# Kernel tuning notes

Hardware: AMD Instinct MI355X
Metric: run time of the kernel (lower is better)

## Reference

```python
import jax, jax.numpy as jnp
import numpy as np

N = 50000      # nodes
E = 800000     # edges
FEAT = 128     # node_feat_size
HID = 128      # hidden_channels
LAT = 64       # latent_size
G = 256        # number of graphs in the batch


def _glorot_like(key, fan_in, shape):
    s = 1.0 / np.sqrt(fan_in)
    return jax.random.uniform(key, shape, jnp.float32, -s, s)


def setup_inputs() -> dict:
    key = jax.random.key(0)
    ks = jax.random.split(key, 13)
    x = jax.random.normal(ks[0], (N, FEAT), jnp.float32)
    edge_index = jax.random.randint(ks[1], (2, E), 0, N, dtype=jnp.int64)
    batch = jnp.sort(jax.random.randint(ks[2], (N,), 0, G, dtype=jnp.int64))
    return {
        "x": x,
        "edge_index": edge_index,
        "batch": batch,
        # GCNConv1: FEAT -> HID
        "W1": _glorot_like(ks[3], FEAT, (FEAT, HID)), "b1": jnp.zeros((HID,), jnp.float32),
        # GCNConv2: HID -> HID
        "W2": _glorot_like(ks[4], HID, (HID, HID)), "b2": jnp.zeros((HID,), jnp.float32),
        # fc: HID -> LAT
        "fcW": _glorot_like(ks[5], HID, (HID, LAT)), "fcb": _glorot_like(ks[6], HID, (LAT,)),
        # decoder: LAT -> HID
        "decW": _glorot_like(ks[7], LAT, (LAT, HID)), "decb": _glorot_like(ks[8], LAT, (HID,)),
        # GCNConv3: HID -> FEAT
        "W3": _glorot_like(ks[9], HID, (HID, FEAT)), "b3": jnp.zeros((FEAT,), jnp.float32),
    }


def reference(x, edge_index, batch, W1, b1, W2, b2, fcW, fcb, decW, decb, W3, b3):
    # --- GCN normalization with self-loops (computed once, shared by all convs) ---
    loop = jnp.arange(N, dtype=edge_index.dtype)
    row = jnp.concatenate([edge_index[0], loop])   # source nodes [E+N]
    col = jnp.concatenate([edge_index[1], loop])   # target nodes [E+N]
    deg = jax.ops.segment_sum(jnp.ones(row.shape, x.dtype), col, num_segments=N)
    dinv = jnp.where(deg > 0, jax.lax.rsqrt(deg), jnp.zeros_like(deg))
    norm = dinv[row] * dinv[col]                   # [E+N]

    def gcn(h, W, b):
        h = h @ W                                   # [N, out] transform first (PyG order)
        msg = h[row] * norm[:, None]                # gather + scale, [E+N, out]
        out = jax.ops.segment_sum(msg, col, num_segments=N)  # scatter-add
        return out + b

    # --- encode ---
    h = jax.nn.relu(gcn(x, W1, b1))
    h = jax.nn.relu(gcn(h, W2, b2))
    pooled = jax.ops.segment_sum(h, batch, num_segments=G)   # global_add_pool [G, HID]
    latent = jax.nn.relu(pooled @ fcW + fcb)                 # [G, LAT]

    # --- decode ---
    z = jax.nn.relu(latent @ decW + decb)                    # [G, HID]
    z = z[batch]                                             # broadcast back to nodes [N, HID]
    recon = gcn(z, W3, b3)                                   # [N, FEAT]
    return recon, latent
```

## Files before the change

kernel.cpp:

```cpp
#include <hip/hip_runtime.h>
#include <hip/hip_fp16.h>

static constexpr int NN   = 50000;
static constexpr int EE   = 800000;
static constexpr int GG   = 256;
static constexpr int PCH  = 16;
static constexpr int BK   = 128;
static constexpr int NB   = (NN + BK - 1) / BK;
static constexpr int CAP  = 4096;
static constexpr int CH   = 2048;
static constexpr int ABLK = (EE + CH - 1) / CH;
static constexpr int PBBB = EE / 64;

typedef _Float16 f16;
typedef f16  f16x8 __attribute__((ext_vector_type(8)));
typedef float f32x4 __attribute__((ext_vector_type(4)));

__device__ __forceinline__ int lowerb(const int* __restrict__ b, int n, int v) {
    int lo = 0, hi = n;
    while (lo < hi) { int m = (lo + hi) >> 1; if (b[m] < v) lo = m + 1; else hi = m; }
    return lo;
}

__device__ __forceinline__ int pack_rec(int bg, float w) {
    __half h = __float2half(w);
    return bg | ((int)__builtin_bit_cast(unsigned short, h) << 16);
}
__device__ __forceinline__ float rec_w(int rec) {
    return __half2float(__builtin_bit_cast(__half, (unsigned short)((unsigned)rec >> 16)));
}

__global__ __launch_bounds__(256) void prep_k(const float* __restrict__ W1,
                                              const float* __restrict__ W2,
                                              f16x8* __restrict__ whi1, f16x8* __restrict__ wlo1,
                                              f16x8* __restrict__ whi2, f16x8* __restrict__ wlo2,
                                              int* __restrict__ bcur,
                                              float* __restrict__ pooled)
{
    int blk = blockIdx.x, t = threadIdx.x;
    if (blk < 16) {
        const float* W = (blk < 8) ? W1 : W2;
        f16x8* wh = (blk < 8) ? whi1 : whi2;
        f16x8* wl = (blk < 8) ? wlo1 : wlo2;
        int tid = (blk & 7) * 256 + t;
        int m  = tid & 15;
        int kq = (tid >> 4) & 3;
        int ks = (tid >> 6) & 3;
        int nt = tid >> 8;
        int n  = nt * 16 + m;
        int k0 = ks * 32 + kq * 8;
        f16x8 h8, l8;
        #pragma unroll
        for (int u = 0; u < 8; u++) {
            float x = W[(size_t)(k0 + u) * 128 + n];
            f16 h = (f16)x;
            h8[u] = h;
            l8[u] = (f16)(x - (float)h);
        }
        wh[tid] = h8;
        wl[tid] = l8;
    } else if (blk == 16) {
        for (int b = t; b < NB; b += 256) bcur[b] = b * CAP;
    } else {
        float4* p = (float4*)pooled;
        for (int j = (blk - 17) * 256 + t; j < GG * 32; j += 512)
            p[j] = make_float4(0.f, 0.f, 0.f, 0.f);
    }
}

__global__ __launch_bounds__(512) void binA_k(const int* __restrict__ ei,
                                              int* __restrict__ bcur,
                                              int2* __restrict__ eraw)
{
    __shared__ int2  stage[CH];
    __shared__ short sbid[CH];
    __shared__ int   hist[NB], loff[NB], gbase[NB], lcur[NB];
    __shared__ int   sc[512];

    int tid = threadIdx.x;
    int e0 = blockIdx.x * CH;
    int n = EE - e0; if (n > CH) n = CH;

    for (int b = tid; b < NB; b += 512) hist[b] = 0;
    __syncthreads();

    int2 r[CH / 512];
    #pragma unroll
    for (int k = 0; k < CH / 512; k++) {
        int s = k * 512 + tid;
        if (s < n) {
            int src = ei[e0 + s];
            int dst = ei[EE + e0 + s];
            r[k] = make_int2(src, dst);
            atomicAdd(&hist[dst >> 7], 1);
        }
    }
    __syncthreads();
    int v = (tid < NB) ? hist[tid] : 0;
    sc[tid] = v;
    __syncthreads();
    #pragma unroll
    for (int off = 1; off < 512; off <<= 1) {
        int add = (tid >= off) ? sc[tid - off] : 0;
        __syncthreads();
        sc[tid] += add;
        __syncthreads();
    }
    if (tid < NB) { int ex = sc[tid] - v; loff[tid] = ex; lcur[tid] = ex; }
    __syncthreads();
    for (int b = tid; b < NB; b += 512)
        gbase[b] = atomicAdd(&bcur[b], hist[b]);
    __syncthreads();
    #pragma unroll
    for (int k = 0; k < CH / 512; k++) {
        int s = k * 512 + tid;
        if (s < n) {
            int b = r[k].y >> 7;
            int slot = atomicAdd(&lcur[b], 1);
            stage[slot] = r[k];
            sbid[slot]  = (short)b;
        }
    }
    __syncthreads();
    for (int s = tid; s < n; s += 512) {
        int b = sbid[s];
        eraw[(size_t)gbase[b] + (s - loff[b])] = stage[s];
    }
}

__global__ __launch_bounds__(512) void binB_k(const int2* __restrict__ eraw,
                                              const int* __restrict__ bcur,
                                              int* __restrict__ rowptr,
                                              float* __restrict__ dinv,
                                              int* __restrict__ ebuf)
{
    __shared__ int hist[BK], excl[BK], cur[BK];
    __shared__ int red[512];
    int b = blockIdx.x, tid = threadIdx.x;
    int t0 = b << 7;
    int lim = NN - t0; if (lim > BK) lim = BK;
    int tot = bcur[b] - b * CAP;

    red[tid] = (tid < b) ? (bcur[tid] - tid * CAP) : 0;
    __syncthreads();
    #pragma unroll
    for (int off = 256; off > 0; off >>= 1) {
        if (tid < off) red[tid] += red[tid + off];
        __syncthreads();
    }
    int base = red[0];
    __syncthreads();

    const int2* er = eraw + (size_t)b * CAP;

    if (tid < BK) hist[tid] = 0;
    __syncthreads();
    for (int s = tid; s < tot; s += 512) atomicAdd(&hist[er[s].y & 127], 1);
    __syncthreads();
    if (tid < BK) excl[tid] = hist[tid];
    __syncthreads();
    #pragma unroll
    for (int off = 1; off < BK; off <<= 1) {
        int add = (tid >= off && tid < BK) ? excl[tid - off] : 0;
        __syncthreads();
        if (tid < BK) excl[tid] += add;
        __syncthreads();
    }
    if (tid < BK) {
        int ex = excl[tid] - hist[tid];
        cur[tid] = base + ex;
        if (tid < lim) {
            rowptr[t0 + tid] = base + ex;
            dinv[t0 + tid]   = rsqrtf((float)(hist[tid] + 1));
        }
    }
    if (b == NB - 1 && tid == 0) rowptr[NN] = EE;
    __syncthreads();
    for (int s = tid; s < tot; s += 512) {
        int2 rec = er[s];
        int p = atomicAdd(&cur[rec.y & 127], 1);
        ebuf[p] = rec.x;
    }
}

__global__ __launch_bounds__(512) void gemm_mfma3_k(const float* __restrict__ in,
                                                    const f16x8* __restrict__ whi_f,
                                                    const f16x8* __restrict__ wlo_f,
                                                    const float* __restrict__ dinv,
                                                    __half* __restrict__ out,
                                                    int rows)
{
    __shared__ __align__(16) f16x8 sh[2048];
    int tid  = threadIdx.x;
    #pragma unroll
    for (int u = 0; u < 4; u++) sh[u * 512 + tid] = whi_f[u * 512 + tid];
    __syncthreads();

    int lane = tid & 63;
    int wv   = tid >> 6;
    int rB   = blockIdx.x * 128 + wv * 16;
    int m    = lane & 15;
    int kq   = lane >> 4;
    int r    = rB + m;
    int rr   = (r < rows) ? r : (rows - 1);

    f16x8 ahi[4], alo[4];
    const float* rp = in + (size_t)rr * 128 + kq * 8;
    #pragma unroll
    for (int ks = 0; ks < 4; ks++) {
        float4 p0 = *(const float4*)(rp + ks * 32);
        float4 p1 = *(const float4*)(rp + ks * 32 + 4);
        float xs[8] = {p0.x, p0.y, p0.z, p0.w, p1.x, p1.y, p1.z, p1.w};
        #pragma unroll
        for (int u = 0; u < 8; u++) {
            f16 h = (f16)xs[u];
            ahi[ks][u] = h;
            alo[ks][u] = (f16)(xs[u] - (float)h);
        }
    }

    f32x4 acc[8];
    #pragma unroll
    for (int n = 0; n < 8; n++) acc[n] = (f32x4){0.f, 0.f, 0.f, 0.f};

    #pragma unroll
    for (int nt = 0; nt < 8; nt++) {
        #pragma unroll
        for (int ks = 0; ks < 4; ks++) {
            int idx = ((nt * 4 + ks) * 4 + kq) * 16 + m;
            f16x8 bh = sh[idx];
            f16x8 bl = wlo_f[idx];
            acc[nt] = __builtin_amdgcn_mfma_f32_16x16x32_f16(ahi[ks], bh, acc[nt], 0, 0, 0);
            acc[nt] = __builtin_amdgcn_mfma_f32_16x16x32_f16(alo[ks], bh, acc[nt], 0, 0, 0);
            acc[nt] = __builtin_amdgcn_mfma_f32_16x16x32_f16(ahi[ks], bl, acc[nt], 0, 0, 0);
        }
    }

    int   orow[4];
    float dv[4];
    #pragma unroll
    for (int j = 0; j < 4; j++) {
        int gr = rB + kq * 4 + j;
        orow[j] = gr;
        dv[j]   = (gr < rows) ? dinv[gr] : 0.f;
    }
    #pragma unroll
    for (int nt = 0; nt < 8; nt++) {
        int c = nt * 16 + m;
        #pragma unroll
        for (int j = 0; j < 4; j++) {
            if (orow[j] < rows)
                out[(size_t)orow[j] * 128 + c] = __float2half(acc[nt][j] * dv[j]);
        }
    }
}

__global__ __launch_bounds__(512) void gemm_mfma2h_k(const __half* __restrict__ in,
                                                     const f16x8* __restrict__ whi_f,
                                                     const f16x8* __restrict__ wlo_f,
                                                     const float* __restrict__ dinv,
                                                     __half* __restrict__ out,
                                                     int rows)
{
    __shared__ __align__(16) f16x8 sh[2048];
    int tid  = threadIdx.x;
    #pragma unroll
    for (int u = 0; u < 4; u++) sh[u * 512 + tid] = whi_f[u * 512 + tid];
    __syncthreads();

    int lane = tid & 63;
    int wv   = tid >> 6;
    int rB   = blockIdx.x * 128 + wv * 16;
    int m    = lane & 15;
    int kq   = lane >> 4;
    int r    = rB + m;
    int rr   = (r < rows) ? r : (rows - 1);

    f16x8 ah[4];
    const f16* rp = (const f16*)in + (size_t)rr * 128 + kq * 8;
    #pragma unroll
    for (int ks = 0; ks < 4; ks++)
        ah[ks] = *(const f16x8*)(rp + ks * 32);

    f32x4 acc[8];
    #pragma unroll
    for (int n = 0; n < 8; n++) acc[n] = (f32x4){0.f, 0.f, 0.f, 0.f};

    #pragma unroll
    for (int nt = 0; nt < 8; nt++) {
        #pragma unroll
        for (int ks = 0; ks < 4; ks++) {
            int idx = ((nt * 4 + ks) * 4 + kq) * 16 + m;
            f16x8 bh = sh[idx];
            f16x8 bl = wlo_f[idx];
            acc[nt] = __builtin_amdgcn_mfma_f32_16x16x32_f16(ah[ks], bh, acc[nt], 0, 0, 0);
            acc[nt] = __builtin_amdgcn_mfma_f32_16x16x32_f16(ah[ks], bl, acc[nt], 0, 0, 0);
        }
    }

    int   orow[4];
    float dv[4];
    #pragma unroll
    for (int j = 0; j < 4; j++) {
        int gr = rB + kq * 4 + j;
        orow[j] = gr;
        dv[j]   = (gr < rows) ? dinv[gr] : 0.f;
    }
    #pragma unroll
    for (int nt = 0; nt < 8; nt++) {
        int c = nt * 16 + m;
        #pragma unroll
        for (int j = 0; j < 4; j++) {
            if (orow[j] < rows)
                out[(size_t)orow[j] * 128 + c] = __float2half(acc[nt][j] * dv[j]);
        }
    }
}

__device__ __forceinline__ float4 gat4h(const __half* __restrict__ t, int s, int q)
{
    uint2 v = *(const uint2*)(t + ((size_t)s << 7) + q * 4);
    __half2 a = __builtin_bit_cast(__half2, v.x);
    __half2 b = __builtin_bit_cast(__half2, v.y);
    float2 fa = __half22float2(a), fb = __half22float2(b);
    return make_float4(fa.x, fa.y, fb.x, fb.y);
}

#define AGG_BODY                                                                 \
    int e0 = __builtin_amdgcn_readfirstlane(rowptr[i]);                          \
    int e1 = __builtin_amdgcn_readfirstlane(rowptr[i + 1]);                      \
    int deg = e1 - e0;                                                           \
    int idxsafe = (deg > 0) ? (e0 + min(lane, deg - 1)) : 0;                     \
    int myidx = ebuf[idxsafe];                                                   \
    float a0 = 0.f, a1 = 0.f, a2 = 0.f, a3 = 0.f;                                \
    if (half == 0) {                                                             \
        float4 v = gat4h(t, i, q);                                               \
        a0 = v.x; a1 = v.y; a2 = v.z; a3 = v.w;                                  \
    }                                                                            \
    int v   = min(deg, 64);                                                      \
    int c16 = v & ~15;                                                           \
    for (int j = half * 8; j < c16; j += 16) {                                   \
        int s0 = __shfl(myidx, j + 0), s1 = __shfl(myidx, j + 1);                \
        int s2 = __shfl(myidx, j + 2), s3 = __shfl(myidx, j + 3);                \
        int s4 = __shfl(myidx, j + 4), s5 = __shfl(myidx, j + 5);                \
        int s6 = __shfl(myidx, j + 6), s7 = __shfl(myidx, j + 7);                \
        float4 w0 = gat4h(t, s0, q);                                             \
        float4 w1 = gat4h(t, s1, q);                                             \
        float4 w2 = gat4h(t, s2, q);                                             \
        float4 w3 = gat4h(t, s3, q);                                             \
        float4 w4 = gat4h(t, s4, q);                                             \
        float4 w5 = gat4h(t, s5, q);                                             \
        float4 w6 = gat4h(t, s6, q);                                             \
        float4 w7 = gat4h(t, s7, q);                                             \
        a0 += w0.x + w1.x + w2.x + w3.x + w4.x + w5.x + w6.x + w7.x;             \
        a1 += w0.y + w1.y + w2.y + w3.y + w4.y + w5.y + w6.y + w7.y;             \
        a2 += w0.z + w1.z + w2.z + w3.z + w4.z + w5.z + w6.z + w7.z;             \
        a3 += w0.w + w1.w + w2.w + w3.w + w4.w + w5.w + w6.w + w7.w;             \
    }                                                                            \
    if (v - c16 >= 8) {                                                          \
        int j = c16 + half * 4;                                                  \
        int s0 = __shfl(myidx, j + 0), s1 = __shfl(myidx, j + 1);                \
        int s2 = __shfl(myidx, j + 2), s3 = __shfl(myidx, j + 3);                \
        float4 w0 = gat4h(t, s0, q);                                             \
        float4 w1 = gat4h(t, s1, q);                                             \
        float4 w2 = gat4h(t, s2, q);                                             \
        float4 w3 = gat4h(t, s3, q);                                             \
        a0 += w0.x + w1.x + w2.x + w3.x;                                         \
        a1 += w0.y + w1.y + w2.y + w3.y;                                         \
        a2 += w0.z + w1.z + w2.z + w3.z;                                         \
        a3 += w0.w + w1.w + w2.w + w3.w;                                         \
    }                                                                            \
    int done = c16 + ((v - c16) & 8);                                            \
    for (int j = done + half; j < v; j += 2) {                                   \
        int s = __shfl(myidx, j);                                                \
        float4 w = gat4h(t, s, q);                                               \
        a0 += w.x; a1 += w.y; a2 += w.z; a3 += w.w;                              \
    }                                                                            \
    for (int e = e0 + 64 + half; e < e1; e += 2) {                               \
        float4 w = gat4h(t, ebuf[e], q);                                         \
        a0 += w.x; a1 += w.y; a2 += w.z; a3 += w.w;                              \
    }                                                                            \
    a0 += __shfl_xor(a0, 32);                                                    \
    a1 += __shfl_xor(a1, 32);                                                    \
    a2 += __shfl_xor(a2, 32);                                                    \
    a3 += __shfl_xor(a3, 32);

__global__ __launch_bounds__(64) void aggh_k(const __half* __restrict__ t,
                                             const int* __restrict__ rowptr,
                                             const int* __restrict__ ebuf,
                                             const float* __restrict__ dinv,
                                             const float* __restrict__ bias,
                                             __half* __restrict__ out,
                                             const int* __restrict__ batch,
                                             int* __restrict__ ebuf2)
{
    int bid  = blockIdx.x;
    int lane = threadIdx.x;
    if (bid >= NN) {
        int e = (bid - NN) * 64 + lane;
        if (e < EE) {
            int src = ebuf[e];
            ebuf2[e] = pack_rec(batch[src], dinv[src]);
        }
        return;
    }
    int i    = bid;
    int half = lane >> 5;
    int q    = lane & 31;
    AGG_BODY
    if (half == 0) {
        float di = dinv[i];
        float4 b = *(const float4*)(bias + q * 4);
        float ox = fmaxf(di * a0 + b.x, 0.f);
        float oy = fmaxf(di * a1 + b.y, 0.f);
        float oz = fmaxf(di * a2 + b.z, 0.f);
        float ow = fmaxf(di * a3 + b.w, 0.f);
        __half2 h01 = __floats2half2_rn(ox, oy);
        __half2 h23 = __floats2half2_rn(oz, ow);
        uint2 u = make_uint2(__builtin_bit_cast(unsigned, h01),
                             __builtin_bit_cast(unsigned, h23));
        *(uint2*)(out + (size_t)i * 128 + q * 4) = u;
    }
}

__global__ __launch_bounds__(64) void agg_out_k(const float* __restrict__ zz,
                                                const int* __restrict__ batch,
                                                const int* __restrict__ rowptr,
                                                const int* __restrict__ ebuf2,
                                                const float* __restrict__ dinv,
                                                const float* __restrict__ bias,
                                                float* __restrict__ out)
{
    int i    = blockIdx.x;
    int lane = threadIdx.x;
    int half = lane >> 5;
    int q    = lane & 31;
    float di = dinv[i];

    float a0 = 0.f, a1 = 0.f, a2 = 0.f, a3 = 0.f;
    if (half == 0) {
        float4 v = *(const float4*)(zz + ((size_t)batch[i] << 7) + q * 4);
        a0 = di * v.x; a1 = di * v.y; a2 = di * v.z; a3 = di * v.w;
    }

    int e0 = rowptr[i], e1 = rowptr[i + 1];
    int deg = e1 - e0;
    int full = deg & ~7;
    int ee = e0 + full;
    for (int e = e0 + half * 4; e < ee; e += 8) {
        int r0 = ebuf2[e],     r1 = ebuf2[e + 1];
        int r2 = ebuf2[e + 2], r3 = ebuf2[e + 3];
        float4 w0 = *(const float4*)(zz + ((size_t)(r0 & 0xffff) << 7) + q * 4);
        float4 w1 = *(const float4*)(zz + ((size_t)(r1 & 0xffff) << 7) + q * 4);
        float4 w2 = *(const float4*)(zz + ((size_t)(r2 & 0xffff) << 7) + q * 4);
        float4 w3 = *(const float4*)(zz + ((size_t)(r3 & 0xffff) << 7) + q * 4);
        float n0 = rec_w(r0), n1 = rec_w(r1);
        float n2 = rec_w(r2), n3 = rec_w(r3);
        a0 += n0 * w0.x + n1 * w1.x + n2 * w2.x + n3 * w3.x;
        a1 += n0 * w0.y + n1 * w1.y + n2 * w2.y + n3 * w3.y;
        a2 += n0 * w0.z + n1 * w1.z + n2 * w2.z + n3 * w3.z;
        a3 += n0 * w0.w + n1 * w1.w + n2 * w2.w + n3 * w3.w;
    }
    for (int e = ee + half; e < e1; e += 2) {
        int r = ebuf2[e];
        float nm = rec_w(r);
        float4 w = *(const float4*)(zz + ((size_t)(r & 0xffff) << 7) + q * 4);
        a0 += nm * w.x; a1 += nm * w.y; a2 += nm * w.z; a3 += nm * w.w;
    }
    a0 += __shfl_xor(a0, 32);
    a1 += __shfl_xor(a1, 32);
    a2 += __shfl_xor(a2, 32);
    a3 += __shfl_xor(a3, 32);

    if (half == 0) {
        float4 b = *(const float4*)(bias + q * 4);
        float4 o;
        o.x = di * a0 + b.x;
        o.y = di * a1 + b.y;
        o.z = di * a2 + b.z;
        o.w = di * a3 + b.w;
        *(float4*)(out + (size_t)i * 128 + q * 4) = o;
    }
}

__global__ __launch_bounds__(128) void pool2_k(const __half* __restrict__ h2,
                                               const int* __restrict__ batch,
                                               float* __restrict__ pooled)
{
    int g = blockIdx.x;
    int c = blockIdx.y;
    int f = threadIdx.x;
    int bs = lowerb(batch, NN, g);
    int be = lowerb(batch, NN, g + 1);
    int len = be - bs;
    int cs = bs + (int)(((long long)len * c) / PCH);
    int ce = bs + (int)(((long long)len * (c + 1)) / PCH);
    float a = 0.f;
    for (int i = cs; i < ce; i++) a += __half2float(h2[(size_t)i * 128 + f]);
    if (ce > cs) atomicAdd(&pooled[(size_t)g * 128 + f], a);
}

__global__ __launch_bounds__(128) void fcdec_k(const float* __restrict__ pooled,
                                               const float* __restrict__ fcW,
                                               const float* __restrict__ fcb,
                                               const float* __restrict__ decW,
                                               const float* __restrict__ decb,
                                               const float* __restrict__ W3,
                                               float* __restrict__ lat_out,
                                               float* __restrict__ zz)
{
    __shared__ float lat[64];
    __shared__ float zs[128];
    int g = blockIdx.x, c = threadIdx.x;
    if (c < 64) {
        const float* p = pooled + (size_t)g * 128;
        float a = fcb[c];
        #pragma unroll 8
        for (int k = 0; k < 128; k++) a = fmaf(p[k], fcW[(size_t)k * 64 + c], a);
        a = fmaxf(a, 0.f);
        lat[c] = a;
        lat_out[(size_t)g * 64 + c] = a;
    }
    __syncthreads();
    {
        float a = decb[c];
        #pragma unroll 8
        for (int k = 0; k < 64; k++) a = fmaf(lat[k], decW[(size_t)k * 128 + c], a);
        zs[c] = fmaxf(a, 0.f);
    }
    __syncthreads();
    float o = 0.f;
    #pragma unroll 8
    for (int k = 0; k < 128; k++) o = fmaf(zs[k], W3[(size_t)k * 128 + c], o);
    zz[(size_t)g * 128 + c] = o;
}

extern "C" void kernel_launch(void* const* d_in, const int* in_sizes, int n_in,
                              void* d_out, int out_size, void* d_ws, size_t ws_size,
                              hipStream_t stream)
{
    const float* x     = (const float*)d_in[0];
    const int*   ei    = (const int*)d_in[1];
    const int*   batch = (const int*)d_in[2];
    const float* W1  = (const float*)d_in[3];
    const float* b1  = (const float*)d_in[4];
    const float* W2  = (const float*)d_in[5];
    const float* b2  = (const float*)d_in[6];
    const float* fcW = (const float*)d_in[7];
    const float* fcb = (const float*)d_in[8];
    const float* decW= (const float*)d_in[9];
    const float* decb= (const float*)d_in[10];
    const float* W3  = (const float*)d_in[11];
    const float* b3  = (const float*)d_in[12];

    char* ws = (char*)d_ws;
    size_t off = 0;
    auto alloc = [&](size_t bytes) -> char* {
        char* p = ws + off;
        off = (off + bytes + 255) & ~(size_t)255;
        return p;
    };
    float* dinv     = (float*)alloc((size_t)NN * 4);
    int*   rowptr   = (int*)alloc((size_t)(NN + 1) * 4);
    int*   bcur     = (int*)alloc((size_t)NB * 4);
    int*   ebuf     = (int*)alloc((size_t)EE * 4);
    int*   ebuf2    = (int*)alloc((size_t)EE * 4);
    float* pooled   = (float*)alloc((size_t)GG * 128 * 4);
    float* zz       = (float*)alloc((size_t)GG * 128 * 4);
    f16x8* whi1     = (f16x8*)alloc(2048 * 16);
    f16x8* wlo1     = (f16x8*)alloc(2048 * 16);
    f16x8* whi2     = (f16x8*)alloc(2048 * 16);
    f16x8* wlo2     = (f16x8*)alloc(2048 * 16);
    __half* A       = (__half*)alloc((size_t)NN * 128 * 2);
    __half* B       = (__half*)alloc((size_t)NN * 128 * 2);
    int2*  eraw     = (int2*)alloc((size_t)NB * CAP * 8);

    float* recon_out = (float*)d_out;
    float* lat_out   = (float*)d_out + (size_t)NN * 128;

    prep_k<<<19, 256, 0, stream>>>(W1, W2, whi1, wlo1, whi2, wlo2, bcur, pooled);
    binA_k<<<ABLK, 512, 0, stream>>>(ei, bcur, eraw);
    binB_k<<<NB, 512, 0, stream>>>(eraw, bcur, rowptr, dinv, ebuf);

    int gblk = (NN + 127) / 128;
    gemm_mfma3_k<<<gblk, 512, 0, stream>>>(x, whi1, wlo1, dinv, A, NN);
    aggh_k<<<NN + PBBB, 64, 0, stream>>>(A, rowptr, ebuf, dinv, b1, B, batch, ebuf2);
    gemm_mfma2h_k<<<gblk, 512, 0, stream>>>(B, whi2, wlo2, dinv, A, NN);
    aggh_k<<<NN, 64, 0, stream>>>(A, rowptr, ebuf, dinv, b2, B, batch, ebuf2);
    pool2_k<<<dim3(GG, PCH), 128, 0, stream>>>(B, batch, pooled);
    fcdec_k<<<GG, 128, 0, stream>>>(pooled, fcW, fcb, decW, decb, W3, lat_out, zz);
    agg_out_k<<<NN, 64, 0, stream>>>(zz, batch, rowptr, ebuf2, dinv,
                                     b3, recon_out);
}
```

Baseline: 266.0 us.

## Fuse first GEMM with edge binning and restructure aggregation gathers via shuffles

The first GEMM no longer depends on dinv, so it is merged into the edge-binning kernel as extra blocks and runs concurrently with binning. The dinv scaling of source rows moves into a new first-layer aggregation kernel, which loads per-edge indices and weights once per wave and broadcasts them with shuffles. The decoder's per-graph table is stored in half precision, and the output aggregation uses the same shuffle-broadcast scheme. This removes one launch and overlaps compute with binning, at the cost of extra half rounding and a per-edge dinv lookup.

Result: faster. 252.2 us (-5.2%).

```diff
diff --git a/kernel.cpp b/kernel.cpp
--- a/kernel.cpp
+++ b/kernel.cpp
@@ -10,6 +10,7 @@
 static constexpr int CAP  = 4096;
 static constexpr int CH   = 2048;
 static constexpr int ABLK = (EE + CH - 1) / CH;
+static constexpr int GBLK = (NN + 127) / 128;
 static constexpr int PBBB = EE / 64;
 
 typedef _Float16 f16;
@@ -68,17 +69,86 @@
     }
 }
 
-__global__ __launch_bounds__(512) void binA_k(const int* __restrict__ ei,
-                                              int* __restrict__ bcur,
-                                              int2* __restrict__ eraw)
-{
-    __shared__ int2  stage[CH];
-    __shared__ short sbid[CH];
-    __shared__ int   hist[NB], loff[NB], gbase[NB], lcur[NB];
-    __shared__ int   sc[512];
-
+__global__ __launch_bounds__(512) void gemm1_binA_k(const float* __restrict__ in,
+                                                    const f16x8* __restrict__ whi_f,
+                                                    const f16x8* __restrict__ wlo_f,
+                                                    __half* __restrict__ out,
+                                                    const int* __restrict__ ei,
+                                                    int* __restrict__ bcur,
+                                                    int2* __restrict__ eraw)
+{
+    __shared__ __align__(16) char smem[32768];
     int tid = threadIdx.x;
-    int e0 = blockIdx.x * CH;
+
+    if (blockIdx.x < GBLK) {
+        f16x8* sh = (f16x8*)smem;
+        #pragma unroll
+        for (int u = 0; u < 4; u++) sh[u * 512 + tid] = whi_f[u * 512 + tid];
+        __syncthreads();
+
+        int lane = tid & 63;
+        int wv   = tid >> 6;
+        int rB   = blockIdx.x * 128 + wv * 16;
+        int m    = lane & 15;
+        int kq   = lane >> 4;
+        int r    = rB + m;
+        int rr   = (r < NN) ? r : (NN - 1);
+
+        f16x8 ahi[4], alo[4];
+        const float* rp = in + (size_t)rr * 128 + kq * 8;
+        #pragma unroll
+        for (int ks = 0; ks < 4; ks++) {
+            float4 p0 = *(const float4*)(rp + ks * 32);
+            float4 p1 = *(const float4*)(rp + ks * 32 + 4);
+            float xs[8] = {p0.x, p0.y, p0.z, p0.w, p1.x, p1.y, p1.z, p1.w};
+            #pragma unroll
+            for (int u = 0; u < 8; u++) {
+                f16 h = (f16)xs[u];
+                ahi[ks][u] = h;
+                alo[ks][u] = (f16)(xs[u] - (float)h);
+            }
+        }
+
+        f32x4 acc[8];
+        #pragma unroll
+        for (int n = 0; n < 8; n++) acc[n] = (f32x4){0.f, 0.f, 0.f, 0.f};
+
+        #pragma unroll
+        for (int nt = 0; nt < 8; nt++) {
+            #pragma unroll
+            for (int ks = 0; ks < 4; ks++) {
+                int idx = ((nt * 4 + ks) * 4 + kq) * 16 + m;
+                f16x8 bh = sh[idx];
+                f16x8 bl = wlo_f[idx];
+                acc[nt] = __builtin_amdgcn_mfma_f32_16x16x32_f16(ahi[ks], bh, acc[nt], 0, 0, 0);
+                acc[nt] = __builtin_amdgcn_mfma_f32_16x16x32_f16(alo[ks], bh, acc[nt], 0, 0, 0);
+                acc[nt] = __builtin_amdgcn_mfma_f32_16x16x32_f16(ahi[ks], bl, acc[nt], 0, 0, 0);
+            }
+        }
+
+        #pragma unroll
+        for (int nt = 0; nt < 8; nt++) {
+            int c = nt * 16 + m;
+            #pragma unroll
+            for (int j = 0; j < 4; j++) {
+                int gr = rB + kq * 4 + j;
+                if (gr < NN)
+                    out[(size_t)gr * 128 + c] = __float2half(acc[nt][j]);
+            }
+        }
+        return;
+    }
+
+    int2*  stage = (int2*)smem;
+    short* sbid  = (short*)(smem + 16384);
+    int*   hist  = (int*)(smem + 20480);
+    int*   loff  = hist + NB;
+    int*   gbase = loff + NB;
+    int*   lcur  = gbase + NB;
+    int*   sc    = (int*)(smem + 26736);
+
+    int b0 = blockIdx.x - GBLK;
+    int e0 = b0 * CH;
     int n = EE - e0; if (n > CH) n = CH;
 
     for (int b = tid; b < NB; b += 512) hist[b] = 0;
@@ -180,78 +250,6 @@
         int2 rec = er[s];
         int p = atomicAdd(&cur[rec.y & 127], 1);
         ebuf[p] = rec.x;
-    }
-}
-
-__global__ __launch_bounds__(512) void gemm_mfma3_k(const float* __restrict__ in,
-                                                    const f16x8* __restrict__ whi_f,
-                                                    const f16x8* __restrict__ wlo_f,
-                                                    const float* __restrict__ dinv,
-                                                    __half* __restrict__ out,
-                                                    int rows)
-{
-    __shared__ __align__(16) f16x8 sh[2048];
-    int tid  = threadIdx.x;
-    #pragma unroll
-    for (int u = 0; u < 4; u++) sh[u * 512 + tid] = whi_f[u * 512 + tid];
-    __syncthreads();
-
-    int lane = tid & 63;
-    int wv   = tid >> 6;
-    int rB   = blockIdx.x * 128 + wv * 16;
-    int m    = lane & 15;
-    int kq   = lane >> 4;
-    int r    = rB + m;
-    int rr   = (r < rows) ? r : (rows - 1);
-
-    f16x8 ahi[4], alo[4];
-    const float* rp = in + (size_t)rr * 128 + kq * 8;
-    #pragma unroll
-    for (int ks = 0; ks < 4; ks++) {
-        float4 p0 = *(const float4*)(rp + ks * 32);
-        float4 p1 = *(const float4*)(rp + ks * 32 + 4);
-        float xs[8] = {p0.x, p0.y, p0.z, p0.w, p1.x, p1.y, p1.z, p1.w};
-        #pragma unroll
-        for (int u = 0; u < 8; u++) {
-            f16 h = (f16)xs[u];
-            ahi[ks][u] = h;
-            alo[ks][u] = (f16)(xs[u] - (float)h);
-        }
-    }
-
-    f32x4 acc[8];
-    #pragma unroll
-    for (int n = 0; n < 8; n++) acc[n] = (f32x4){0.f, 0.f, 0.f, 0.f};
-
-    #pragma unroll
-    for (int nt = 0; nt < 8; nt++) {
-        #pragma unroll
-        for (int ks = 0; ks < 4; ks++) {
-            int idx = ((nt * 4 + ks) * 4 + kq) * 16 + m;
-            f16x8 bh = sh[idx];
-            f16x8 bl = wlo_f[idx];
-            acc[nt] = __builtin_amdgcn_mfma_f32_16x16x32_f16(ahi[ks], bh, acc[nt], 0, 0, 0);
-            acc[nt] = __builtin_amdgcn_mfma_f32_16x16x32_f16(alo[ks], bh, acc[nt], 0, 0, 0);
-            acc[nt] = __builtin_amdgcn_mfma_f32_16x16x32_f16(ahi[ks], bl, acc[nt], 0, 0, 0);
-        }
-    }
-
-    int   orow[4];
-    float dv[4];
-    #pragma unroll
-    for (int j = 0; j < 4; j++) {
-        int gr = rB + kq * 4 + j;
-        orow[j] = gr;
-        dv[j]   = (gr < rows) ? dinv[gr] : 0.f;
-    }
-    #pragma unroll
-    for (int nt = 0; nt < 8; nt++) {
-        int c = nt * 16 + m;
-        #pragma unroll
-        for (int j = 0; j < 4; j++) {
-            if (orow[j] < rows)
-                out[(size_t)orow[j] * 128 + c] = __float2half(acc[nt][j] * dv[j]);
-        }
     }
 }
 
@@ -423,7 +421,119 @@
     }
 }
 
-__global__ __launch_bounds__(64) void agg_out_k(const float* __restrict__ zz,
+__global__ __launch_bounds__(64) void agghw_k(const __half* __restrict__ t,
+                                              const int* __restrict__ rowptr,
+                                              const int* __restrict__ ebuf,
+                                              const float* __restrict__ dinv,
+                                              const float* __restrict__ bias,
+                                              __half* __restrict__ out,
+                                              const int* __restrict__ batch,
+                                              int* __restrict__ ebuf2)
+{
+    int bid  = blockIdx.x;
+    int lane = threadIdx.x;
+    if (bid >= NN) {
+        int e = (bid - NN) * 64 + lane;
+        if (e < EE) {
+            int src = ebuf[e];
+            ebuf2[e] = pack_rec(batch[src], dinv[src]);
+        }
+        return;
+    }
+    int i    = bid;
+    int half = lane >> 5;
+    int q    = lane & 31;
+    float di = dinv[i];
+
+    int e0 = __builtin_amdgcn_readfirstlane(rowptr[i]);
+    int e1 = __builtin_amdgcn_readfirstlane(rowptr[i + 1]);
+    int deg = e1 - e0;
+    int idxsafe = (deg > 0) ? (e0 + min(lane, deg - 1)) : 0;
+    int myidx = ebuf[idxsafe];
+    float myw = dinv[myidx];
+
+    float a0 = 0.f, a1 = 0.f, a2 = 0.f, a3 = 0.f;
+    if (half == 0) {
+        float4 sv = gat4h(t, i, q);
+        a0 = di * sv.x; a1 = di * sv.y; a2 = di * sv.z; a3 = di * sv.w;
+    }
+
+    int v   = min(deg, 64);
+    int c16 = v & ~15;
+    for (int j = half * 8; j < c16; j += 16) {
+        int s0 = __shfl(myidx, j + 0), s1 = __shfl(myidx, j + 1);
+        int s2 = __shfl(myidx, j + 2), s3 = __shfl(myidx, j + 3);
+        int s4 = __shfl(myidx, j + 4), s5 = __shfl(myidx, j + 5);
+        int s6 = __shfl(myidx, j + 6), s7 = __shfl(myidx, j + 7);
+        float n0 = __shfl(myw, j + 0), n1 = __shfl(myw, j + 1);
+        float n2 = __shfl(myw, j + 2), n3 = __shfl(myw, j + 3);
+        float n4 = __shfl(myw, j + 4), n5 = __shfl(myw, j + 5);
+        float n6 = __shfl(myw, j + 6), n7 = __shfl(myw, j + 7);
+        float4 w0 = gat4h(t, s0, q);
+        float4 w1 = gat4h(t, s1, q);
+        float4 w2 = gat4h(t, s2, q);
+        float4 w3 = gat4h(t, s3, q);
+        float4 w4 = gat4h(t, s4, q);
+        float4 w5 = gat4h(t, s5, q);
+        float4 w6 = gat4h(t, s6, q);
+        float4 w7 = gat4h(t, s7, q);
+        a0 += n0 * w0.x + n1 * w1.x + n2 * w2.x + n3 * w3.x
+            + n4 * w4.x + n5 * w5.x + n6 * w6.x + n7 * w7.x;
+        a1 += n0 * w0.y + n1 * w1.y + n2 * w2.y + n3 * w3.y
+            + n4 * w4.y + n5 * w5.y + n6 * w6.y + n7 * w7.y;
+        a2 += n0 * w0.z + n1 * w1.z + n2 * w2.z + n3 * w3.z
+            + n4 * w4.z + n5 * w5.z + n6 * w6.z + n7 * w7.z;
+        a3 += n0 * w0.w + n1 * w1.w + n2 * w2.w + n3 * w3.w
+            + n4 * w4.w + n5 * w5.w + n6 * w6.w + n7 * w7.w;
+    }
+    if (v - c16 >= 8) {
+        int j = c16 + half * 4;
+        int s0 = __shfl(myidx, j + 0), s1 = __shfl(myidx, j + 1);
+        int s2 = __shfl(myidx, j + 2), s3 = __shfl(myidx, j + 3);
+        float n0 = __shfl(myw, j + 0), n1 = __shfl(myw, j + 1);
+        float n2 = __shfl(myw, j + 2), n3 = __shfl(myw, j + 3);
+        float4 w0 = gat4h(t, s0, q);
+        float4 w1 = gat4h(t, s1, q);
+        float4 w2 = gat4h(t, s2, q);
+        float4 w3 = gat4h(t, s3, q);
+        a0 += n0 * w0.x + n1 * w1.x + n2 * w2.x + n3 * w3.x;
+        a1 += n0 * w0.y + n1 * w1.y + n2 * w2.y + n3 * w3.y;
+        a2 += n0 * w0.z + n1 * w1.z + n2 * w2.z + n3 * w3.z;
+        a3 += n0 * w0.w + n1 * w1.w + n2 * w2.w + n3 * w3.w;
+    }
+    int done = c16 + ((v - c16) & 8);
+    for (int j = done + half; j < v; j += 2) {
+        int s = __shfl(myidx, j);
+        float nm = __shfl(myw, j);
+        float4 w = gat4h(t, s, q);
+        a0 += nm * w.x; a1 += nm * w.y; a2 += nm * w.z; a3 += nm * w.w;
+    }
+    for (int e = e0 + 64 + half; e < e1; e += 2) {
+        int s = ebuf[e];
+        float nm = dinv[s];
+        float4 w = gat4h(t, s, q);
+        a0 += nm * w.x; a1 += nm * w.y; a2 += nm * w.z; a3 += nm * w.w;
+    }
+    a0 += __shfl_xor(a0, 32);
+    a1 += __shfl_xor(a1, 32);
+    a2 += __shfl_xor(a2, 32);
+    a3 += __shfl_xor(a3, 32);
+
+    if (half == 0) {
+        float4 b = *(const float4*)(bias + q * 4);
+        float ox = fmaxf(di * a0 + b.x, 0.f);
+        float oy = fmaxf(di * a1 + b.y, 0.f);
+        float oz = fmaxf(di * a2 + b.z, 0.f);
+        float ow = fmaxf(di * a3 + b.w, 0.f);
+        __half2 h01 = __floats2half2_rn(ox, oy);
+        __half2 h23 = __floats2half2_rn(oz, ow);
+        uint2 u = make_uint2(__builtin_bit_cast(unsigned, h01),
+                             __builtin_bit_cast(unsigned, h23));
+        *(uint2*)(out + (size_t)i * 128 + q * 4) = u;
+    }
+}
+
+__global__ __launch_bounds__(64) void agg_out_k(const __half* __restrict__ zzh,
                                                 const int* __restrict__ batch,
                                                 const int* __restrict__ rowptr,
                                                 const int* __restrict__ ebuf2,
@@ -437,34 +547,69 @@
     int q    = lane & 31;
     float di = dinv[i];
 
+    int e0 = __builtin_amdgcn_readfirstlane(rowptr[i]);
+    int e1 = __builtin_amdgcn_readfirstlane(rowptr[i + 1]);
+    int deg = e1 - e0;
+    int idxsafe = (deg > 0) ? (e0 + min(lane, deg - 1)) : 0;
+    int myrec = ebuf2[idxsafe];
+
     float a0 = 0.f, a1 = 0.f, a2 = 0.f, a3 = 0.f;
     if (half == 0) {
-        float4 v = *(const float4*)(zz + ((size_t)batch[i] << 7) + q * 4);
-        a0 = di * v.x; a1 = di * v.y; a2 = di * v.z; a3 = di * v.w;
-    }
-
-    int e0 = rowptr[i], e1 = rowptr[i + 1];
-    int deg = e1 - e0;
-    int full = deg & ~7;
-    int ee = e0 + full;
-    for (int e = e0 + half * 4; e < ee; e += 8) {
-        int r0 = ebuf2[e],     r1 = ebuf2[e + 1];
-        int r2 = ebuf2[e + 2], r3 = ebuf2[e + 3];
-        float4 w0 = *(const float4*)(zz + ((size_t)(r0 & 0xffff) << 7) + q * 4);
-        float4 w1 = *(const float4*)(zz + ((size_t)(r1 & 0xffff) << 7) + q * 4);
-        float4 w2 = *(const float4*)(zz + ((size_t)(r2 & 0xffff) << 7) + q * 4);
-        float4 w3 = *(const float4*)(zz + ((size_t)(r3 & 0xffff) << 7) + q * 4);
-        float n0 = rec_w(r0), n1 = rec_w(r1);
-        float n2 = rec_w(r2), n3 = rec_w(r3);
+        float4 sv = gat4h(zzh, batch[i], q);
+        a0 = di * sv.x; a1 = di * sv.y; a2 = di * sv.z; a3 = di * sv.w;
+    }
+
+    int v   = min(deg, 64);
+    int c16 = v & ~15;
+    for (int j = half * 8; j < c16; j += 16) {
+        int r0 = __shfl(myrec, j + 0), r1 = __shfl(myrec, j + 1);
+        int r2 = __shfl(myrec, j + 2), r3 = __shfl(myrec, j + 3);
+        int r4 = __shfl(myrec, j + 4), r5 = __shfl(myrec, j + 5);
+        int r6 = __shfl(myrec, j + 6), r7 = __shfl(myrec, j + 7);
+        float4 w0 = gat4h(zzh, r0 & 0xffff, q);
+        float4 w1 = gat4h(zzh, r1 & 0xffff, q);
+        float4 w2 = gat4h(zzh, r2 & 0xffff, q);
+        float4 w3 = gat4h(zzh, r3 & 0xffff, q);
+        float4 w4 = gat4h(zzh, r4 & 0xffff, q);
+        float4 w5 = gat4h(zzh, r5 & 0xffff, q);
+        float4 w6 = gat4h(zzh, r6 & 0xffff, q);
+        float4 w7 = gat4h(zzh, r7 & 0xffff, q);
+        float n0 = rec_w(r0), n1 = rec_w(r1), n2 = rec_w(r2), n3 = rec_w(r3);
+        float n4 = rec_w(r4), n5 = rec_w(r5), n6 = rec_w(r6), n7 = rec_w(r7);
+        a0 += n0 * w0.x + n1 * w1.x + n2 * w2.x + n3 * w3.x
+            + n4 * w4.x + n5 * w5.x + n6 * w6.x + n7 * w7.x;
+        a1 += n0 * w0.y + n1 * w1.y + n2 * w2.y + n3 * w3.y
+            + n4 * w4.y + n5 * w5.y + n6 * w6.y + n7 * w7.y;
+        a2 += n0 * w0.z + n1 * w1.z + n2 * w2.z + n3 * w3.z
+            + n4 * w4.z + n5 * w5.z + n6 * w6.z + n7 * w7.z;
+        a3 += n0 * w0.w + n1 * w1.w + n2 * w2.w + n3 * w3.w
+            + n4 * w4.w + n5 * w5.w + n6 * w6.w + n7 * w7.w;
+    }
+    if (v - c16 >= 8) {
+        int j = c16 + half * 4;
+        int r0 = __shfl(myrec, j + 0), r1 = __shfl(myrec, j + 1);
+        int r2 = __shfl(myrec, j + 2), r3 = __shfl(myrec, j + 3);
+        float4 w0 = gat4h(zzh, r0 & 0xffff, q);
+        float4 w1 = gat4h(zzh, r1 & 0xffff, q);
+        float4 w2 = gat4h(zzh, r2 & 0xffff, q);
+        float4 w3 = gat4h(zzh, r3 & 0xffff, q);
+        float n0 = rec_w(r0), n1 = rec_w(r1), n2 = rec_w(r2), n3 = rec_w(r3);
         a0 += n0 * w0.x + n1 * w1.x + n2 * w2.x + n3 * w3.x;
         a1 += n0 * w0.y + n1 * w1.y + n2 * w2.y + n3 * w3.y;
         a2 += n0 * w0.z + n1 * w1.z + n2 * w2.z + n3 * w3.z;
         a3 += n0 * w0.w + n1 * w1.w + n2 * w2.w + n3 * w3.w;
     }
-    for (int e = ee + half; e < e1; e += 2) {
-        int r = ebuf2[e];
-        float nm = rec_w(r);
-        float4 w = *(const float4*)(zz + ((size_t)(r & 0xffff) << 7) + q * 4);
+    int done = c16 + ((v - c16) & 8);
+    for (int j = done + half; j < v; j += 2) {
+        int rr = __shfl(myrec, j);
+        float nm = rec_w(rr);
+        float4 w = gat4h(zzh, rr & 0xffff, q);
+        a0 += nm * w.x; a1 += nm * w.y; a2 += nm * w.z; a3 += nm * w.w;
+    }
+    for (int e = e0 + 64 + half; e < e1; e += 2) {
+        int rr = ebuf2[e];
+        float nm = rec_w(rr);
+        float4 w = gat4h(zzh, rr & 0xffff, q);
         a0 += nm * w.x; a1 += nm * w.y; a2 += nm * w.z; a3 += nm * w.w;
     }
     a0 += __shfl_xor(a0, 32);
@@ -507,7 +652,7 @@
                                                const float* __restrict__ decb,
                                                const float* __restrict__ W3,
                                                float* __restrict__ lat_out,
-                                               float* __restrict__ zz)
+                                               __half* __restrict__ zzh)
 {
     __shared__ float lat[64];
     __shared__ float zs[128];
@@ -532,7 +677,7 @@
     float o = 0.f;
     #pragma unroll 8
     for (int k = 0; k < 128; k++) o = fmaf(zs[k], W3[(size_t)k * 128 + c], o);
-    zz[(size_t)g * 128 + c] = o;
+    zzh[(size_t)g * 128 + c] = __float2half(o);
 }
 
 extern "C" void kernel_launch(void* const* d_in, const int* in_sizes, int n_in,
@@ -566,7 +711,7 @@
     int*   ebuf     = (int*)alloc((size_t)EE * 4);
     int*   ebuf2    = (int*)alloc((size_t)EE * 4);
     float* pooled   = (float*)alloc((size_t)GG * 128 * 4);
-    float* zz       = (float*)alloc((size_t)GG * 128 * 4);
+    __half* zzh     = (__half*)alloc((size_t)GG * 128 * 2);
     f16x8* whi1     = (f16x8*)alloc(2048 * 16);
     f16x8* wlo1     = (f16x8*)alloc(2048 * 16);
     f16x8* whi2     = (f16x8*)alloc(2048 * 16);
@@ -579,16 +724,14 @@
     float* lat_out   = (float*)d_out + (size_t)NN * 128;
 
     prep_k<<<19, 256, 0, stream>>>(W1, W2, whi1, wlo1, whi2, wlo2, bcur, pooled);
-    binA_k<<<ABLK, 512, 0, stream>>>(ei, bcur, eraw);
+    gemm1_binA_k<<<GBLK + ABLK, 512, 0, stream>>>(x, whi1, wlo1, A, ei, bcur, eraw);
     binB_k<<<NB, 512, 0, stream>>>(eraw, bcur, rowptr, dinv, ebuf);
 
-    int gblk = (NN + 127) / 128;
-    gemm_mfma3_k<<<gblk, 512, 0, stream>>>(x, whi1, wlo1, dinv, A, NN);
-    aggh_k<<<NN + PBBB, 64, 0, stream>>>(A, rowptr, ebuf, dinv, b1, B, batch, ebuf2);
-    gemm_mfma2h_k<<<gblk, 512, 0, stream>>>(B, whi2, wlo2, dinv, A, NN);
+    agghw_k<<<NN + PBBB, 64, 0, stream>>>(A, rowptr, ebuf, dinv, b1, B, batch, ebuf2);
+    gemm_mfma2h_k<<<GBLK, 512, 0, stream>>>(B, whi2, wlo2, dinv, A, NN);
     aggh_k<<<NN, 64, 0, stream>>>(A, rowptr, ebuf, dinv, b2, B, batch, ebuf2);
     pool2_k<<<dim3(GG, PCH), 128, 0, stream>>>(B, batch, pooled);
-    fcdec_k<<<GG, 128, 0, stream>>>(pooled, fcW, fcb, decW, decb, W3, lat_out, zz);
-    agg_out_k<<<NN, 64, 0, stream>>>(zz, batch, rowptr, ebuf2, dinv,
+    fcdec_k<<<GG, 128, 0, stream>>>(pooled, fcW, fcb, decW, decb, W3, lat_out, zzh);
+    agg_out_k<<<NN, 64, 0, stream>>>(zzh, batch, rowptr, ebuf2, dinv,
                                      b3, recon_out);
 }
```
